# Performance work log

Hardware: AMD Instinct MI355X
Metric: run time of the kernel (lower is better)

## Reference

```python
import jax, jax.numpy as jnp
import numpy as np

KH, KW = 3, 3
STRIDE, PAD, DIL = 1, 1, 1
DG = 1  # deformable groups


def setup_inputs() -> dict:
    key = jax.random.key(0)
    k1, k2, k3, k4 = jax.random.split(key, 4)
    B, C, H, W, O = 4, 64, 128, 128, 64
    x = jax.random.normal(k1, (B, C, H, W), jnp.float32)
    weight = jax.random.normal(k2, (O, C, KH, KW), jnp.float32) * 0.05
    bias = jnp.zeros((O,), jnp.float32)
    # offset/mask conv params (zero-init in original; small random here so
    # the bilinear sampling path is actually exercised)
    om_weight = jax.random.normal(k3, (DG * 3 * KH * KW, C, KH, KW), jnp.float32) * 0.01
    om_bias = jax.random.normal(k4, (DG * 3 * KH * KW,), jnp.float32) * 0.01
    return {"x": x, "weight": weight, "bias": bias,
            "om_weight": om_weight, "om_bias": om_bias}


def _dcn(x, weight, bias, om_weight, om_bias):
    B, C, H, W = x.shape
    O = weight.shape[0]
    K = KH * KW
    Cg = C // DG

    # --- offset/mask conv (plain conv2d) ---
    om = jax.lax.conv_general_dilated(
        x, om_weight, (STRIDE, STRIDE), [(PAD, PAD), (PAD, PAD)],
        dimension_numbers=("NCHW", "OIHW", "NCHW"))
    om = om + om_bias[None, :, None, None]
    Ho, Wo = om.shape[2], om.shape[3]
    o1, o2, m = jnp.split(om, 3, axis=1)            # each (B, DG*K, Ho, Wo)
    off_y = o1.reshape(B, DG, K, Ho, Wo)
    off_x = o2.reshape(B, DG, K, Ho, Wo)
    mask = jax.nn.sigmoid(m).reshape(B, DG, K, Ho, Wo)

    # --- fractional sampling positions per kernel tap ---
    ky = jnp.repeat(jnp.arange(KH), KW).astype(jnp.float32)   # (K,)
    kx = jnp.tile(jnp.arange(KW), KH).astype(jnp.float32)
    base_y = (jnp.arange(Ho, dtype=jnp.float32) * STRIDE - PAD)
    base_x = (jnp.arange(Wo, dtype=jnp.float32) * STRIDE - PAD)
    py = off_y + base_y[None, None, None, :, None] + (ky * DIL)[None, None, :, None, None]
    px = off_x + base_x[None, None, None, None, :] + (kx * DIL)[None, None, :, None, None]

    y0 = jnp.floor(py)
    x0 = jnp.floor(px)
    ly = py - y0
    lx = px - x0
    y0i = y0.astype(jnp.int32)
    x0i = x0.astype(jnp.int32)

    xg = x.reshape(B, DG, Cg, H * W)
    # gather spatial samples per (batch, group), broadcast over channels
    gather = jax.vmap(jax.vmap(lambda feat, idx: jnp.take(feat, idx, axis=-1)))

    def corner(yc, xc, w):
        valid = (yc >= 0) & (yc < H) & (xc >= 0) & (xc < W)
        idx = jnp.clip(yc, 0, H - 1) * W + jnp.clip(xc, 0, W - 1)  # (B,DG,K,Ho,Wo)
        v = gather(xg, idx.reshape(B, DG, -1)).reshape(B, DG, Cg, K, Ho, Wo)
        w = jnp.where(valid, w, 0.0)
        return v * w[:, :, None]  # zero-padded bilinear corner

    val = (corner(y0i,     x0i,     (1 - ly) * (1 - lx))
         + corner(y0i,     x0i + 1, (1 - ly) * lx)
         + corner(y0i + 1, x0i,     ly * (1 - lx))
         + corner(y0i + 1, x0i + 1, ly * lx))
    val = val * mask[:, :, None]                    # (B,DG,Cg,K,Ho,Wo)

    w4 = weight.reshape(O, DG, Cg, K)
    out = jnp.einsum("ogck,bgckhw->bohw", w4, val) + bias[None, :, None, None]
    return out


def reference(x, weight, bias, om_weight, om_bias):
    return _dcn(x, weight, bias, om_weight, om_bias)
```

## Files before the change

kernel.cpp:

```cpp
#include <hip/hip_runtime.h>
#include <hip/hip_fp16.h>
#include <math.h>

#define BB 4
#define CC 64
#define HH 128
#define WW 128
#define OO 64
#define HWW (HH * WW)

typedef _Float16 f16x8 __attribute__((ext_vector_type(8)));
typedef float f32x4 __attribute__((ext_vector_type(4)));

#define WHF_OFF  0
#define WLF_OFF  73728
#define WOMH_OFF 147456
#define WOML_OFF 184320

__device__ inline __half2 u2h(unsigned u) {
    union { unsigned u; __half2 h; } c; c.u = u; return c.h;
}
__device__ inline unsigned h2u(__half2 h) {
    union { __half2 h; unsigned u; } c; c.h = h; return c.u;
}

__global__ void prep_kernel(const float* __restrict__ weight,
                            const float* __restrict__ om_weight,
                            unsigned short* __restrict__ whf,
                            unsigned short* __restrict__ wlf,
                            unsigned short* __restrict__ womh,
                            unsigned short* __restrict__ woml)
{
    int d = blockIdx.x * 256 + threadIdx.x;
    if (d < 18 * 4 * 64 * 8) {
        int j  = d & 7;
        int l  = (d >> 3) & 63;
        int wv = (d >> 9) & 3;
        int ch = d >> 11;
        int o  = wv * 16 + (l & 15);
        int kk = (l >> 4) * 8 + j;
        int c  = (ch / 9) * 32 + kk;
        int tap = ch % 9;
        float w = weight[(o * CC + c) * 9 + tap];
        __half h = __float2half_rn(w);
        __half lo = __float2half_rn(w - __half2float(h));
        whf[d] = __half_as_ushort(h);
        wlf[d] = __half_as_ushort(lo);
    }
    int d2 = d - 18 * 4 * 64 * 8;
    if (d2 >= 0 && d2 < 18 * 2 * 64 * 8) {
        int j  = d2 & 7;
        int l  = (d2 >> 3) & 63;
        int og = (d2 >> 9) & 1;
        int ch = d2 >> 10;
        int o  = og * 16 + (l & 15);
        int kk = (l >> 4) * 8 + j;
        int c  = (ch / 9) * 32 + kk;
        int tap = ch % 9;
        float w = (o < 27) ? om_weight[(o * CC + c) * 9 + tap] : 0.f;
        __half h = __float2half_rn(w);
        __half lo = __float2half_rn(w - __half2float(h));
        womh[d2] = __half_as_ushort(h);
        woml[d2] = __half_as_ushort(lo);
    }
}

__global__ void __launch_bounds__(256, 4)
fused_kernel(const float* __restrict__ x,
             const unsigned short* __restrict__ whf,
             const unsigned short* __restrict__ wlf,
             const unsigned short* __restrict__ womh,
             const unsigned short* __restrict__ woml,
             const float* __restrict__ bias,
             const float* __restrict__ om_bias,
             float* __restrict__ out)
{
    __shared__ __align__(16) uint2 Xf[16 * 180];
    __shared__ __align__(16) unsigned vhf[2][32][21];
    __shared__ __align__(16) uint4 swth4[288];
    __shared__ int sidx[288];

    int t    = threadIdx.x;
    int lane = t & 63;
    int wv   = t >> 6;

    int bid = blockIdx.x;
    int b   = bid >> 9;
    int r   = bid & 511;
    int ho  = r >> 2;
    int w0  = (r & 3) << 5;

    {
        const float* xb = x + (size_t)b * CC * HWW;
#pragma unroll 1
        for (int i = t; i < 16 * 180; i += 256) {
            int cg  = i / 180;
            int pos = i - cg * 180;
            int rr  = pos / 36;
            int cc2 = pos - rr * 36;
            int gy = ho - 2 + rr, gx = w0 - 2 + cc2;
            bool ok = (gy >= 0) & (gy < HH) & (gx >= 0) & (gx < WW);
            int gi = ok ? gy * WW + gx : 0;
            const float* xc = xb + (size_t)cg * 4 * HWW + gi;
            float v0 = xc[0], v1 = xc[HWW], v2 = xc[2 * HWW], v3 = xc[3 * HWW];
            if (!ok) { v0 = 0.f; v1 = 0.f; v2 = 0.f; v3 = 0.f; }
            uint2 p;
            p.x = h2u(__floats2half2_rn(v0, v1));
            p.y = h2u(__floats2half2_rn(v2, v3));
            Xf[cg * 180 + pos] = p;
        }
    }
    __syncthreads();

    f32x4 accom = (f32x4){0.f, 0.f, 0.f, 0.f};
    {
        int og = wv & 1;
        int s  = wv >> 1;
        int pix_s = s * 16 + (lane & 15);
#pragma unroll 1
        for (int ch = 0; ch < 18; ch++) {
            int half = ch / 9;
            int tap  = ch - half * 9;
            int cg0  = half * 8 + (lane >> 4) * 2;
            int ky = tap / 3, kx = tap - ky * 3;
            int pos = (ky + 1) * 36 + pix_s + kx + 1;
            uint2 pa = Xf[cg0 * 180 + pos];
            uint2 pb = Xf[(cg0 + 1) * 180 + pos];
            union { f16x8 v; unsigned u[4]; } B;
            B.u[0] = pa.x; B.u[1] = pa.y; B.u[2] = pb.x; B.u[3] = pb.y;
            const f16x8 ah = *(const f16x8*)&womh[((size_t)(ch * 2 + og) * 64 + lane) * 8];
            const f16x8 al = *(const f16x8*)&woml[((size_t)(ch * 2 + og) * 64 + lane) * 8];
            accom = __builtin_amdgcn_mfma_f32_16x16x32_f16(ah, B.v, accom, 0, 0, 0);
            accom = __builtin_amdgcn_mfma_f32_16x16x32_f16(al, B.v, accom, 0, 0, 0);
        }
    }

    float* omL = (float*)&vhf[0][0][0];
    {
        int og = wv & 1, s = wv >> 1;
#pragma unroll
        for (int rg = 0; rg < 4; rg++) {
            int m = og * 16 + (lane >> 4) * 4 + rg;
            if (m < 27) {
                int pp = s * 16 + (lane & 15);
                float v = accom[rg] + om_bias[m];
                if (m >= 18) v = 1.f / (1.f + expf(-v));
                omL[m * 32 + pp] = v;
            }
        }
    }
    __syncthreads();

#pragma unroll 1
    for (int it = t; it < 288; it += 256) {
        int k  = it >> 5;
        int pp = it & 31;
        float oy = omL[k * 32 + pp];
        float ox = omL[(9 + k) * 32 + pp];
        float mm = omL[(18 + k) * 32 + pp];
        int ky = k / 3, kx = k - ky * 3;
        float py = oy + (float)(ho + ky - 1);
        float px = ox + (float)(w0 + pp + kx - 1);
        float fy = floorf(py), fx = floorf(px);
        float ly = py - fy, lx = px - fx;
        int y0 = (int)fy, x0 = (int)fx;
        bool vy0 = (y0 >= 0) & (y0 < HH);
        bool vy1 = (y0 + 1 >= 0) & (y0 + 1 < HH);
        bool vx0 = (x0 >= 0) & (x0 < WW);
        bool vx1 = (x0 + 1 >= 0) & (x0 + 1 < WW);
        float w00 = (vy0 & vx0) ? (1.f - ly) * (1.f - lx) * mm : 0.f;
        float w01 = (vy0 & vx1) ? (1.f - ly) * lx * mm : 0.f;
        float w10 = (vy1 & vx0) ? ly * (1.f - lx) * mm : 0.f;
        float w11 = (vy1 & vx1) ? ly * lx * mm : 0.f;
        uint4 wp;
        wp.x = h2u(__float2half2_rn(w00));
        wp.y = h2u(__float2half2_rn(w01));
        wp.z = h2u(__float2half2_rn(w10));
        wp.w = h2u(__float2half2_rn(w11));
        swth4[it] = wp;
        bool inw = (y0 >= ho - 2) & (y0 <= ho + 1) & (x0 >= w0 - 2) & (x0 <= w0 + 32);
        int y0c = min(max(y0, -8), 135);
        int x0c = min(max(x0, -8), 135);
        sidx[it] = ((y0c + 16) << 16) | ((x0c + 16) & 0xFFFF)
                 | (inw ? 0 : (int)0x80000000);
    }
    __syncthreads();

    f32x4 acc[2];
    acc[0] = (f32x4){0.f, 0.f, 0.f, 0.f};
    acc[1] = (f32x4){0.f, 0.f, 0.f, 0.f};

    {
        int pix = t & 31;
        int cg  = t >> 5;
#pragma unroll 1
        for (int ach = 0; ach < 18; ach++) {
            int half = ach / 9;
            int tap  = ach - half * 9;
            int buf  = ach & 1;
            int cgg  = half * 8 + cg;
            const uint2* Xrow = &Xf[cgg * 180];
            int item = tap * 32 + pix;
            uint4 wp = swth4[item];
            int sv = sidx[item];
            int y0 = ((sv >> 16) & 0x7FFF) - 16;
            int x0 = (sv & 0xFFFF) - 16;
            const f16x8 ah = *(const f16x8*)&whf[((size_t)(ach * 4 + wv) * 64 + lane) * 8];
            const f16x8 al = *(const f16x8*)&wlf[((size_t)(ach * 4 + wv) * 64 + lane) * 8];

            uint2 hw;
            if (sv >= 0) {
                int o00 = (y0 - ho + 2) * 36 + (x0 - w0 + 2);
                uint2 c00 = Xrow[o00];
                uint2 c01 = Xrow[o00 + 1];
                uint2 c10 = Xrow[o00 + 36];
                uint2 c11 = Xrow[o00 + 37];
                __half2 w00 = u2h(wp.x), w01 = u2h(wp.y);
                __half2 w10 = u2h(wp.z), w11 = u2h(wp.w);
                __half2 vA = __hmul2(w00, u2h(c00.x));
                vA = __hfma2(w01, u2h(c01.x), vA);
                vA = __hfma2(w10, u2h(c10.x), vA);
                vA = __hfma2(w11, u2h(c11.x), vA);
                __half2 vB = __hmul2(w00, u2h(c00.y));
                vB = __hfma2(w01, u2h(c01.y), vB);
                vB = __hfma2(w10, u2h(c10.y), vB);
                vB = __hfma2(w11, u2h(c11.y), vB);
                hw.x = h2u(vA);
                hw.y = h2u(vB);
            } else {
                const float* xg = x + ((size_t)(b * CC + half * 32 + cg * 4)) * HWW;
                float w00f = __low2float(u2h(wp.x)), w01f = __low2float(u2h(wp.y));
                float w10f = __low2float(u2h(wp.z)), w11f = __low2float(u2h(wp.w));
                int cy0 = min(max(y0, 0), HH - 1), cy1 = min(max(y0 + 1, 0), HH - 1);
                int cx0 = min(max(x0, 0), WW - 1), cx1 = min(max(x0 + 1, 0), WW - 1);
                int i00 = cy0 * WW + cx0, i01 = cy0 * WW + cx1;
                int i10 = cy1 * WW + cx0, i11 = cy1 * WW + cx1;
                float v0 = w00f * xg[i00] + w01f * xg[i01] + w10f * xg[i10] + w11f * xg[i11];
                const float* x1p = xg + HWW;
                float v1 = w00f * x1p[i00] + w01f * x1p[i01] + w10f * x1p[i10] + w11f * x1p[i11];
                const float* x2p = xg + 2 * HWW;
                float v2 = w00f * x2p[i00] + w01f * x2p[i01] + w10f * x2p[i10] + w11f * x2p[i11];
                const float* x3p = xg + 3 * HWW;
                float v3 = w00f * x3p[i00] + w01f * x3p[i01] + w10f * x3p[i10] + w11f * x3p[i11];
                hw.x = h2u(__floats2half2_rn(v0, v1));
                hw.y = h2u(__floats2half2_rn(v2, v3));
            }
            *(uint2*)&vhf[buf][pix][cg * 2] = hw;
            __syncthreads();
#pragma unroll
            for (int s2 = 0; s2 < 2; s2++) {
                union { f16x8 v; unsigned u[4]; } B;
                const unsigned* src = &vhf[buf][s2 * 16 + (lane & 15)][(lane >> 4) * 4];
                B.u[0] = src[0]; B.u[1] = src[1]; B.u[2] = src[2]; B.u[3] = src[3];
                acc[s2] = __builtin_amdgcn_mfma_f32_16x16x32_f16(ah, B.v, acc[s2], 0, 0, 0);
                acc[s2] = __builtin_amdgcn_mfma_f32_16x16x32_f16(al, B.v, acc[s2], 0, 0, 0);
            }
        }
    }

    int prow = ho * WW + w0;
#pragma unroll
    for (int s = 0; s < 2; s++) {
#pragma unroll
        for (int rg = 0; rg < 4; rg++) {
            int o  = wv * 16 + (lane >> 4) * 4 + rg;
            int pp = s * 16 + (lane & 15);
            out[((size_t)(b * OO + o)) * HWW + prow + pp] = acc[s][rg] + bias[o];
        }
    }
}

extern "C" void kernel_launch(void* const* d_in, const int* in_sizes, int n_in,
                              void* d_out, int out_size, void* d_ws, size_t ws_size,
                              hipStream_t stream)
{
    (void)in_sizes; (void)n_in; (void)out_size; (void)ws_size;
    const float* x      = (const float*)d_in[0];
    const float* weight = (const float*)d_in[1];
    const float* bias   = (const float*)d_in[2];
    const float* om_w   = (const float*)d_in[3];
    const float* om_b   = (const float*)d_in[4];
    float* out = (float*)d_out;
    char*  ws  = (char*)d_ws;

    unsigned short* whf  = (unsigned short*)(ws + WHF_OFF);
    unsigned short* wlf  = (unsigned short*)(ws + WLF_OFF);
    unsigned short* womh = (unsigned short*)(ws + WOMH_OFF);
    unsigned short* woml = (unsigned short*)(ws + WOML_OFF);

    int prep_n = 18 * 4 * 64 * 8 + 18 * 2 * 64 * 8;
    prep_kernel<<<(prep_n + 255) / 256, 256, 0, stream>>>(weight, om_w, whf, wlf, womh, woml);

    int nblk = BB * HH * (WW / 32);
    fused_kernel<<<nblk, 256, 0, stream>>>(x, whf, wlf, womh, woml, bias, om_b, out);
}
```

Baseline: 128.7 us.

## Pack 8 channels per LDS entry and process both channel halves per tap

Changes the shared-memory input tile from 4-channel uint2 entries to 8-channel uint4 entries, so the offset conv reads one 16-byte entry per MFMA operand. The deformable sampling loop now runs 9 iterations instead of 18: each thread interpolates 8 channels per sample and each wave issues four MFMAs per tap, halving the number of __syncthreads and bilinear-index setups. The cost is more registers for the weight fragments and per-thread payload, and wider LDS accesses that may change bank-conflict behaviour.

```diff
diff --git a/kernel.cpp b/kernel.cpp
--- a/kernel.cpp
+++ b/kernel.cpp
@@ -75,8 +75,8 @@
              const float* __restrict__ om_bias,
              float* __restrict__ out)
 {
-    __shared__ __align__(16) uint2 Xf[16 * 180];
-    __shared__ __align__(16) unsigned vhf[2][32][21];
+    __shared__ __align__(16) uint4 Xw[8 * 180];
+    __shared__ __align__(16) uint4 vex[2][32][9];
     __shared__ __align__(16) uint4 swth4[288];
     __shared__ int sidx[288];
 
@@ -93,7 +93,7 @@
     {
         const float* xb = x + (size_t)b * CC * HWW;
 #pragma unroll 1
-        for (int i = t; i < 16 * 180; i += 256) {
+        for (int i = t; i < 8 * 180; i += 256) {
             int cg  = i / 180;
             int pos = i - cg * 180;
             int rr  = pos / 36;
@@ -101,13 +101,16 @@
             int gy = ho - 2 + rr, gx = w0 - 2 + cc2;
             bool ok = (gy >= 0) & (gy < HH) & (gx >= 0) & (gx < WW);
             int gi = ok ? gy * WW + gx : 0;
-            const float* xc = xb + (size_t)cg * 4 * HWW + gi;
-            float v0 = xc[0], v1 = xc[HWW], v2 = xc[2 * HWW], v3 = xc[3 * HWW];
-            if (!ok) { v0 = 0.f; v1 = 0.f; v2 = 0.f; v3 = 0.f; }
-            uint2 p;
+            const float* xc = xb + (size_t)cg * 8 * HWW + gi;
+            float v0 = xc[0],       v1 = xc[HWW],     v2 = xc[2 * HWW], v3 = xc[3 * HWW];
+            float v4 = xc[4 * HWW], v5 = xc[5 * HWW], v6 = xc[6 * HWW], v7 = xc[7 * HWW];
+            if (!ok) { v0=0.f; v1=0.f; v2=0.f; v3=0.f; v4=0.f; v5=0.f; v6=0.f; v7=0.f; }
+            uint4 p;
             p.x = h2u(__floats2half2_rn(v0, v1));
             p.y = h2u(__floats2half2_rn(v2, v3));
-            Xf[cg * 180 + pos] = p;
+            p.z = h2u(__floats2half2_rn(v4, v5));
+            p.w = h2u(__floats2half2_rn(v6, v7));
+            Xw[cg * 180 + pos] = p;
         }
     }
     __syncthreads();
@@ -117,17 +120,15 @@
         int og = wv & 1;
         int s  = wv >> 1;
         int pix_s = s * 16 + (lane & 15);
+        int oct   = lane >> 4;
 #pragma unroll 1
         for (int ch = 0; ch < 18; ch++) {
             int half = ch / 9;
             int tap  = ch - half * 9;
-            int cg0  = half * 8 + (lane >> 4) * 2;
             int ky = tap / 3, kx = tap - ky * 3;
             int pos = (ky + 1) * 36 + pix_s + kx + 1;
-            uint2 pa = Xf[cg0 * 180 + pos];
-            uint2 pb = Xf[(cg0 + 1) * 180 + pos];
-            union { f16x8 v; unsigned u[4]; } B;
-            B.u[0] = pa.x; B.u[1] = pa.y; B.u[2] = pb.x; B.u[3] = pb.y;
+            uint4 pw = Xw[(half * 4 + oct) * 180 + pos];
+            union { f16x8 v; uint4 u; } B; B.u = pw;
             const f16x8 ah = *(const f16x8*)&womh[((size_t)(ch * 2 + og) * 64 + lane) * 8];
             const f16x8 al = *(const f16x8*)&woml[((size_t)(ch * 2 + og) * 64 + lane) * 8];
             accom = __builtin_amdgcn_mfma_f32_16x16x32_f16(ah, B.v, accom, 0, 0, 0);
@@ -135,7 +136,7 @@
         }
     }
 
-    float* omL = (float*)&vhf[0][0][0];
+    float* omL = (float*)&vex[0][0][0];
     {
         int og = wv & 1, s = wv >> 1;
 #pragma unroll
@@ -194,27 +195,26 @@
         int pix = t & 31;
         int cg  = t >> 5;
 #pragma unroll 1
-        for (int ach = 0; ach < 18; ach++) {
-            int half = ach / 9;
-            int tap  = ach - half * 9;
-            int buf  = ach & 1;
-            int cgg  = half * 8 + cg;
-            const uint2* Xrow = &Xf[cgg * 180];
+        for (int tap = 0; tap < 9; tap++) {
+            int buf  = tap & 1;
             int item = tap * 32 + pix;
             uint4 wp = swth4[item];
             int sv = sidx[item];
             int y0 = ((sv >> 16) & 0x7FFF) - 16;
             int x0 = (sv & 0xFFFF) - 16;
-            const f16x8 ah = *(const f16x8*)&whf[((size_t)(ach * 4 + wv) * 64 + lane) * 8];
-            const f16x8 al = *(const f16x8*)&wlf[((size_t)(ach * 4 + wv) * 64 + lane) * 8];
-
-            uint2 hw;
+            const f16x8 ah0 = *(const f16x8*)&whf[((size_t)(tap * 4 + wv) * 64 + lane) * 8];
+            const f16x8 al0 = *(const f16x8*)&wlf[((size_t)(tap * 4 + wv) * 64 + lane) * 8];
+            const f16x8 ah1 = *(const f16x8*)&whf[((size_t)((9 + tap) * 4 + wv) * 64 + lane) * 8];
+            const f16x8 al1 = *(const f16x8*)&wlf[((size_t)((9 + tap) * 4 + wv) * 64 + lane) * 8];
+
+            uint4 payload;
             if (sv >= 0) {
                 int o00 = (y0 - ho + 2) * 36 + (x0 - w0 + 2);
-                uint2 c00 = Xrow[o00];
-                uint2 c01 = Xrow[o00 + 1];
-                uint2 c10 = Xrow[o00 + 36];
-                uint2 c11 = Xrow[o00 + 37];
+                const uint4* Xrow = &Xw[cg * 180];
+                uint4 c00 = Xrow[o00];
+                uint4 c01 = Xrow[o00 + 1];
+                uint4 c10 = Xrow[o00 + 36];
+                uint4 c11 = Xrow[o00 + 37];
                 __half2 w00 = u2h(wp.x), w01 = u2h(wp.y);
                 __half2 w10 = u2h(wp.z), w11 = u2h(wp.w);
                 __half2 vA = __hmul2(w00, u2h(c00.x));
@@ -225,35 +225,47 @@
                 vB = __hfma2(w01, u2h(c01.y), vB);
                 vB = __hfma2(w10, u2h(c10.y), vB);
                 vB = __hfma2(w11, u2h(c11.y), vB);
-                hw.x = h2u(vA);
-                hw.y = h2u(vB);
+                __half2 vC = __hmul2(w00, u2h(c00.z));
+                vC = __hfma2(w01, u2h(c01.z), vC);
+                vC = __hfma2(w10, u2h(c10.z), vC);
+                vC = __hfma2(w11, u2h(c11.z), vC);
+                __half2 vD = __hmul2(w00, u2h(c00.w));
+                vD = __hfma2(w01, u2h(c01.w), vD);
+                vD = __hfma2(w10, u2h(c10.w), vD);
+                vD = __hfma2(w11, u2h(c11.w), vD);
+                payload.x = h2u(vA); payload.y = h2u(vB);
+                payload.z = h2u(vC); payload.w = h2u(vD);
             } else {
-                const float* xg = x + ((size_t)(b * CC + half * 32 + cg * 4)) * HWW;
+                const float* xg = x + ((size_t)(b * CC + cg * 8)) * HWW;
                 float w00f = __low2float(u2h(wp.x)), w01f = __low2float(u2h(wp.y));
                 float w10f = __low2float(u2h(wp.z)), w11f = __low2float(u2h(wp.w));
                 int cy0 = min(max(y0, 0), HH - 1), cy1 = min(max(y0 + 1, 0), HH - 1);
                 int cx0 = min(max(x0, 0), WW - 1), cx1 = min(max(x0 + 1, 0), WW - 1);
                 int i00 = cy0 * WW + cx0, i01 = cy0 * WW + cx1;
                 int i10 = cy1 * WW + cx0, i11 = cy1 * WW + cx1;
-                float v0 = w00f * xg[i00] + w01f * xg[i01] + w10f * xg[i10] + w11f * xg[i11];
-                const float* x1p = xg + HWW;
-                float v1 = w00f * x1p[i00] + w01f * x1p[i01] + w10f * x1p[i10] + w11f * x1p[i11];
-                const float* x2p = xg + 2 * HWW;
-                float v2 = w00f * x2p[i00] + w01f * x2p[i01] + w10f * x2p[i10] + w11f * x2p[i11];
-                const float* x3p = xg + 3 * HWW;
-                float v3 = w00f * x3p[i00] + w01f * x3p[i01] + w10f * x3p[i10] + w11f * x3p[i11];
-                hw.x = h2u(__floats2half2_rn(v0, v1));
-                hw.y = h2u(__floats2half2_rn(v2, v3));
+                float vv[8];
+#pragma unroll
+                for (int j = 0; j < 8; j++) {
+                    const float* xc = xg + (size_t)j * HWW;
+                    vv[j] = w00f * xc[i00] + w01f * xc[i01]
+                          + w10f * xc[i10] + w11f * xc[i11];
+                }
+                payload.x = h2u(__floats2half2_rn(vv[0], vv[1]));
+                payload.y = h2u(__floats2half2_rn(vv[2], vv[3]));
+                payload.z = h2u(__floats2half2_rn(vv[4], vv[5]));
+                payload.w = h2u(__floats2half2_rn(vv[6], vv[7]));
             }
-            *(uint2*)&vhf[buf][pix][cg * 2] = hw;
+            vex[buf][pix][cg] = payload;
             __syncthreads();
 #pragma unroll
             for (int s2 = 0; s2 < 2; s2++) {
-                union { f16x8 v; unsigned u[4]; } B;
-                const unsigned* src = &vhf[buf][s2 * 16 + (lane & 15)][(lane >> 4) * 4];
-                B.u[0] = src[0]; B.u[1] = src[1]; B.u[2] = src[2]; B.u[3] = src[3];
-                acc[s2] = __builtin_amdgcn_mfma_f32_16x16x32_f16(ah, B.v, acc[s2], 0, 0, 0);
-                acc[s2] = __builtin_amdgcn_mfma_f32_16x16x32_f16(al, B.v, acc[s2], 0, 0, 0);
+                union { f16x8 v; uint4 u; } B0, B1;
+                B0.u = vex[buf][s2 * 16 + (lane & 15)][lane >> 4];
+                B1.u = vex[buf][s2 * 16 + (lane & 15)][4 + (lane >> 4)];
+                acc[s2] = __builtin_amdgcn_mfma_f32_16x16x32_f16(ah0, B0.v, acc[s2], 0, 0, 0);
+                acc[s2] = __builtin_amdgcn_mfma_f32_16x16x32_f16(al0, B0.v, acc[s2], 0, 0, 0);
+                acc[s2] = __builtin_amdgcn_mfma_f32_16x16x32_f16(ah1, B1.v, acc[s2], 0, 0, 0);
+                acc[s2] = __builtin_amdgcn_mfma_f32_16x16x32_f16(al1, B1.v, acc[s2], 0, 0, 0);
             }
         }
     }
```

New measurement: 119.8 us. 6.9% less time.
